# Optimization experiments

Measured on AMD Instinct MI355X. Metric: run time of the kernel, lower is better.

The kernel has to match this reference:

```python
import jax, jax.numpy as jnp
import numpy as np

N_ATOMS = 100000
N_EDGES = 6400000

def setup_inputs() -> dict:
    key = jax.random.key(0)
    k1, k2, k3 = jax.random.split(key, 3)
    R = jax.random.normal(k1, (N_ATOMS, 3), dtype=jnp.float32)
    idx_i = jax.random.randint(k2, (N_EDGES,), 0, N_ATOMS, dtype=jnp.int64)
    idx_j = jax.random.randint(k3, (N_EDGES,), 0, N_ATOMS, dtype=jnp.int64)
    return {"R": R, "idx_i": idx_i, "idx_j": idx_j}

def reference(R, idx_i, idx_j):
    # Gather coordinates at both ends of each edge, subtract, L2 norm over xyz.
    Rij = R[idx_i] - R[idx_j]            # [E, 3]
    d_ij = jnp.sqrt(jnp.sum(Rij * Rij, axis=-1))  # [E]
    return d_ij
```

## Files before the change

kernel.cpp:

```cpp
#include <hip/hip_runtime.h>
#include <hip/hip_bf16.h>


__global__ __launch_bounds__(256) void pairwise_dist_kernel(
    const float* __restrict__ R,
    const int* __restrict__ idx_i,
    const int* __restrict__ idx_j,
    float* __restrict__ out,
    int n_edges)
{
    const int quad = blockIdx.x * blockDim.x + threadIdx.x;
    const int n_quads = n_edges >> 2;

    if (quad < n_quads) {
        const int4 a = ((const int4*)idx_i)[quad];
        const int4 b = ((const int4*)idx_j)[quad];

        float4 o;
        {
            const float* pa = R + 3 * (long)a.x;
            const float* pb = R + 3 * (long)b.x;
            float dx = pa[0] - pb[0], dy = pa[1] - pb[1], dz = pa[2] - pb[2];
            o.x = sqrtf(dx * dx + dy * dy + dz * dz);
        }
        {
            const float* pa = R + 3 * (long)a.y;
            const float* pb = R + 3 * (long)b.y;
            float dx = pa[0] - pb[0], dy = pa[1] - pb[1], dz = pa[2] - pb[2];
            o.y = sqrtf(dx * dx + dy * dy + dz * dz);
        }
        {
            const float* pa = R + 3 * (long)a.z;
            const float* pb = R + 3 * (long)b.z;
            float dx = pa[0] - pb[0], dy = pa[1] - pb[1], dz = pa[2] - pb[2];
            o.z = sqrtf(dx * dx + dy * dy + dz * dz);
        }
        {
            const float* pa = R + 3 * (long)a.w;
            const float* pb = R + 3 * (long)b.w;
            float dx = pa[0] - pb[0], dy = pa[1] - pb[1], dz = pa[2] - pb[2];
            o.w = sqrtf(dx * dx + dy * dy + dz * dz);
        }
        ((float4*)out)[quad] = o;
    }

    const int tail_start = n_quads << 2;
    const int tail = n_edges - tail_start;
    if (tail > 0 && quad < tail) {
        const int e = tail_start + quad;
        const int ia = idx_i[e], ib = idx_j[e];
        const float* pa = R + 3 * (long)ia;
        const float* pb = R + 3 * (long)ib;
        float dx = pa[0] - pb[0], dy = pa[1] - pb[1], dz = pa[2] - pb[2];
        out[e] = sqrtf(dx * dx + dy * dy + dz * dz);
    }
}

extern "C" void kernel_launch(void* const* d_in, const int* in_sizes, int n_in,
                              void* d_out, int out_size, void* d_ws, size_t ws_size,
                              hipStream_t stream)
{
    const float* R     = (const float*)d_in[0];
    const int*   idx_i = (const int*)d_in[1];
    const int*   idx_j = (const int*)d_in[2];
    float*       out   = (float*)d_out;

    const int n_edges = in_sizes[1];
    const int n_quads = (n_edges + 3) >> 2;
    const int block   = 256;
    const int grid    = (n_quads + block - 1) / block;

    pairwise_dist_kernel<<<grid, block, 0, stream>>>(R, idx_i, idx_j, out, n_edges);
}
```

Before: 143.9 us.

## Pad coordinates to float4 in workspace and use nontemporal streaming loads/stores

Adds a pre-pass that copies R into a 16-byte-aligned xyz0 layout in the workspace, so each gathered atom becomes a single 128-bit load instead of three scalar loads. Index reads and the output write now use nontemporal builtins, to keep the streamed data from evicting the cached coordinate table. The tail handling moves to a separate kernel. The trade-off is an extra kernel launch plus a 1.6 MB workspace write, and a larger table footprint (from 1.2 MB to 1.6 MB).

```diff
diff --git a/kernel.cpp b/kernel.cpp
--- a/kernel.cpp
+++ b/kernel.cpp
@@ -2,57 +2,77 @@
 #include <hip/hip_bf16.h>
 
 
+typedef int   v4i __attribute__((ext_vector_type(4)));
+typedef float v4f __attribute__((ext_vector_type(4)));
+
+__global__ __launch_bounds__(256) void pad_R_kernel(
+    const float* __restrict__ R, float* __restrict__ R4, int n_atoms)
+{
+    const int i = blockIdx.x * blockDim.x + threadIdx.x;
+    if (i < n_atoms) {
+        const float x = R[3 * i + 0];
+        const float y = R[3 * i + 1];
+        const float z = R[3 * i + 2];
+        v4f v = {x, y, z, 0.0f};
+        *(v4f*)(R4 + 4 * (size_t)i) = v;
+    }
+}
+
 __global__ __launch_bounds__(256) void pairwise_dist_kernel(
-    const float* __restrict__ R,
+    const float* __restrict__ R4,
     const int* __restrict__ idx_i,
     const int* __restrict__ idx_j,
     float* __restrict__ out,
-    int n_edges)
+    int n_quads)
 {
     const int quad = blockIdx.x * blockDim.x + threadIdx.x;
-    const int n_quads = n_edges >> 2;
+    if (quad >= n_quads) return;
 
-    if (quad < n_quads) {
-        const int4 a = ((const int4*)idx_i)[quad];
-        const int4 b = ((const int4*)idx_j)[quad];
+    const v4i a = __builtin_nontemporal_load((const v4i*)idx_i + quad);
+    const v4i b = __builtin_nontemporal_load((const v4i*)idx_j + quad);
 
-        float4 o;
-        {
-            const float* pa = R + 3 * (long)a.x;
-            const float* pb = R + 3 * (long)b.x;
-            float dx = pa[0] - pb[0], dy = pa[1] - pb[1], dz = pa[2] - pb[2];
-            o.x = sqrtf(dx * dx + dy * dy + dz * dz);
-        }
-        {
-            const float* pa = R + 3 * (long)a.y;
-            const float* pb = R + 3 * (long)b.y;
-            float dx = pa[0] - pb[0], dy = pa[1] - pb[1], dz = pa[2] - pb[2];
-            o.y = sqrtf(dx * dx + dy * dy + dz * dz);
-        }
-        {
-            const float* pa = R + 3 * (long)a.z;
-            const float* pb = R + 3 * (long)b.z;
-            float dx = pa[0] - pb[0], dy = pa[1] - pb[1], dz = pa[2] - pb[2];
-            o.z = sqrtf(dx * dx + dy * dy + dz * dz);
-        }
-        {
-            const float* pa = R + 3 * (long)a.w;
-            const float* pb = R + 3 * (long)b.w;
-            float dx = pa[0] - pb[0], dy = pa[1] - pb[1], dz = pa[2] - pb[2];
-            o.w = sqrtf(dx * dx + dy * dy + dz * dz);
-        }
-        ((float4*)out)[quad] = o;
+    const v4f pa0 = *(const v4f*)(R4 + 4 * (size_t)a.x);
+    const v4f pb0 = *(const v4f*)(R4 + 4 * (size_t)b.x);
+    const v4f pa1 = *(const v4f*)(R4 + 4 * (size_t)a.y);
+    const v4f pb1 = *(const v4f*)(R4 + 4 * (size_t)b.y);
+    const v4f pa2 = *(const v4f*)(R4 + 4 * (size_t)a.z);
+    const v4f pb2 = *(const v4f*)(R4 + 4 * (size_t)b.z);
+    const v4f pa3 = *(const v4f*)(R4 + 4 * (size_t)a.w);
+    const v4f pb3 = *(const v4f*)(R4 + 4 * (size_t)b.w);
+
+    v4f o;
+    {
+        const v4f d = pa0 - pb0;
+        o.x = sqrtf(d.x * d.x + d.y * d.y + d.z * d.z);
     }
+    {
+        const v4f d = pa1 - pb1;
+        o.y = sqrtf(d.x * d.x + d.y * d.y + d.z * d.z);
+    }
+    {
+        const v4f d = pa2 - pb2;
+        o.z = sqrtf(d.x * d.x + d.y * d.y + d.z * d.z);
+    }
+    {
+        const v4f d = pa3 - pb3;
+        o.w = sqrtf(d.x * d.x + d.y * d.y + d.z * d.z);
+    }
+    __builtin_nontemporal_store(o, (v4f*)out + quad);
+}
 
-    const int tail_start = n_quads << 2;
-    const int tail = n_edges - tail_start;
-    if (tail > 0 && quad < tail) {
-        const int e = tail_start + quad;
-        const int ia = idx_i[e], ib = idx_j[e];
-        const float* pa = R + 3 * (long)ia;
-        const float* pb = R + 3 * (long)ib;
-        float dx = pa[0] - pb[0], dy = pa[1] - pb[1], dz = pa[2] - pb[2];
-        out[e] = sqrtf(dx * dx + dy * dy + dz * dz);
+__global__ __launch_bounds__(64) void pairwise_dist_tail_kernel(
+    const float* __restrict__ R4,
+    const int* __restrict__ idx_i,
+    const int* __restrict__ idx_j,
+    float* __restrict__ out,
+    int start, int n_edges)
+{
+    const int e = start + blockIdx.x * blockDim.x + threadIdx.x;
+    if (e < n_edges) {
+        const v4f pa = *(const v4f*)(R4 + 4 * (size_t)idx_i[e]);
+        const v4f pb = *(const v4f*)(R4 + 4 * (size_t)idx_j[e]);
+        const v4f d = pa - pb;
+        out[e] = sqrtf(d.x * d.x + d.y * d.y + d.z * d.z);
     }
 }
 
@@ -65,10 +85,27 @@
     const int*   idx_j = (const int*)d_in[2];
     float*       out   = (float*)d_out;
 
+    const int n_atoms = in_sizes[0] / 3;
     const int n_edges = in_sizes[1];
-    const int n_quads = (n_edges + 3) >> 2;
-    const int block   = 256;
-    const int grid    = (n_quads + block - 1) / block;
+    float*    R4      = (float*)d_ws;
 
-    pairwise_dist_kernel<<<grid, block, 0, stream>>>(R, idx_i, idx_j, out, n_edges);
+    {
+        const int block = 256;
+        const int grid  = (n_atoms + block - 1) / block;
+        pad_R_kernel<<<grid, block, 0, stream>>>(R, R4, n_atoms);
+    }
+
+    const int n_quads = n_edges >> 2;
+    {
+        const int block = 256;
+        const int grid  = (n_quads + block - 1) / block;
+        pairwise_dist_kernel<<<grid, block, 0, stream>>>(R4, idx_i, idx_j, out, n_quads);
+    }
+
+    const int tail_start = n_quads << 2;
+    if (tail_start < n_edges) {
+        const int tail = n_edges - tail_start;
+        pairwise_dist_tail_kernel<<<(tail + 63) / 64, 64, 0, stream>>>(
+            R4, idx_i, idx_j, out, tail_start, n_edges);
+    }
 }
```

Measured after the change: 152.7 us. 1.06x slower.
